# Kernel optimization log

Hardware: AMD Instinct MI355X
Metric: run time of the kernel (lower is better)

Reference implementation:

```python
import jax, jax.numpy as jnp
import numpy as np

B, T, IN, H = 1024, 200, 128, 128

def _linear_params(key, out_dim, in_dim):
    kw, kb = jax.random.split(key)
    bound = 1.0 / np.sqrt(in_dim)
    w = jax.random.uniform(kw, (out_dim, in_dim), jnp.float32, -bound, bound)
    b = jax.random.uniform(kb, (out_dim,), jnp.float32, -bound, bound)
    return w, b

def setup_inputs() -> dict:
    key = jax.random.key(0)
    ks = jax.random.split(key, 10)
    targets = jax.random.normal(ks[0], (B, T, IN), jnp.float32)
    history_states = jax.random.normal(ks[1], (B, T, H), jnp.float32)
    W_w, W_b = _linear_params(ks[2], H, IN)
    xu_w, xu_b = _linear_params(ks[3], H, H)
    hu_w, hu_b = _linear_params(ks[4], H, H)
    xr_w, xr_b = _linear_params(ks[5], H, H)
    hr_w, hr_b = _linear_params(ks[6], H, H)
    xg_w, xg_b = _linear_params(ks[7], H, H)
    hg_w, hg_b = _linear_params(ks[8], H, H)
    ln2_w, ln2_b = _linear_params(ks[9], H, IN + H)
    return dict(targets=targets, history_states=history_states,
                W_w=W_w, W_b=W_b, xu_w=xu_w, xu_b=xu_b, hu_w=hu_w, hu_b=hu_b,
                xr_w=xr_w, xr_b=xr_b, hr_w=hr_w, hr_b=hr_b,
                xg_w=xg_w, xg_b=xg_b, hg_w=hg_w, hg_b=hg_b,
                ln2_w=ln2_w, ln2_b=ln2_b)

def reference(targets, history_states, W_w, W_b, xu_w, xu_b, hu_w, hu_b,
              xr_w, xr_b, hr_w, hr_b, xg_w, xg_b, hg_w, hg_b, ln2_w, ln2_b):
    # attention weights: softmax over time of <W(targets), history>
    aw = jnp.einsum('bti,hi->bth', targets, W_w) + W_b            # [B,T,H]
    att = jax.nn.softmax(jnp.sum(aw * history_states, -1, keepdims=True), axis=1)  # [B,T,1]

    # precompute input-side projections as big GEMMs (same math as per-step Linear)
    xu = jnp.einsum('bth,oh->bto', history_states, xu_w) + xu_b   # [B,T,H]
    xr = jnp.einsum('bth,oh->bto', history_states, xr_w) + xr_b
    xg = jnp.einsum('bth,oh->bto', history_states, xg_w) + xg_b

    def step(h, xs):
        xu_t, xr_t, xg_t, a_t = xs                                 # [B,H],[B,H],[B,H],[B,1]
        u = jax.nn.sigmoid(xu_t + h @ hu_w.T + hu_b) * a_t
        r = jax.nn.sigmoid(xr_t + h @ hr_w.T + hr_b)
        g = jnp.tanh(xg_t + r * (h @ hg_w.T + hg_b))
        h = (1.0 - u) * h + u * g
        return h, None

    h0 = jnp.zeros((targets.shape[0], hu_w.shape[0]), targets.dtype)
    # scan over time: move T to leading axis
    xs = (jnp.swapaxes(xu, 0, 1), jnp.swapaxes(xr, 0, 1),
          jnp.swapaxes(xg, 0, 1), jnp.swapaxes(att, 0, 1))
    h, _ = jax.lax.scan(step, h0, xs)

    out = jnp.concatenate([h, targets[:, 0]], axis=-1) @ ln2_w.T + ln2_b
    return out
```

## Files before the change

### kernel.cpp

```cpp
#include <hip/hip_runtime.h>

#define B_ 1024
#define T_ 200
#define H_ 128

typedef __attribute__((ext_vector_type(8))) short short8;
typedef __attribute__((ext_vector_type(4))) float f32x4;

#define MFMA(a, b, c) __builtin_amdgcn_mfma_f32_16x16x32_bf16((a), (b), (c), 0, 0, 0)

static __device__ __forceinline__ short f2bf(float f) {
  unsigned u = __float_as_uint(f);
  u += 0x7fffu + ((u >> 16) & 1u);
  return (short)(u >> 16);
}
static __device__ __forceinline__ float bf2f(short s) {
  return __uint_as_float(((unsigned)(unsigned short)s) << 16);
}
static __device__ __forceinline__ unsigned pack2bf_rne(float a, float b) {
  unsigned ua = __float_as_uint(a);
  ua += 0x7fffu + ((ua >> 16) & 1u);
  unsigned ub = __float_as_uint(b);
  ub += 0x7fffu + ((ub >> 16) & 1u);
  return (ua >> 16) | (ub & 0xFFFF0000u);
}
static __device__ __forceinline__ unsigned pack2bf_trunc(float a, float b) {
  return (__float_as_uint(a) >> 16) | (__float_as_uint(b) & 0xFFFF0000u);
}
static __device__ __forceinline__ float rcp_f(float x) { return __builtin_amdgcn_rcpf(x); }
static __device__ __forceinline__ void ck_barrier() {
  asm volatile("s_waitcnt lgkmcnt(0)\n\ts_barrier" ::: "memory");
}

__global__ __launch_bounds__(512, 1) void proj_scores_kernel(
    const float* __restrict__ tgt, const float* __restrict__ hist,
    const float* __restrict__ Ww, const float* __restrict__ Wb,
    float* __restrict__ scores, short* __restrict__ histbf) {
  const int tc = blockIdx.x, bb = blockIdx.y;
  const int nt = (tc == 12) ? 8 : 16;
  const int t0 = tc * 16;
  const int tid = threadIdx.x;
  const int lane = tid & 63, w = tid >> 6;
  const int n = lane & 15, q = lane >> 4;

  __shared__ short tgt_hi[2][16 * 128];
  __shared__ short tgt_lo[2][16 * 128];
  __shared__ float hist_f[2][16 * 132];
  __shared__ float sp[16 * 8];

  short8 whi[4], wlo[4];
  f32x4 wb4;
  {
    const int o = w * 16 + n;
#pragma unroll
    for (int ks = 0; ks < 4; ++ks) {
      const float* p = Ww + o * H_ + ks * 32 + q * 8;
      short8 h, l;
#pragma unroll
      for (int j = 0; j < 8; ++j) {
        float f = p[j];
        short hv = f2bf(f);
        h[j] = hv;
        l[j] = f2bf(f - bf2f(hv));
      }
      whi[ks] = h;
      wlo[ks] = l;
    }
    wb4 = *(const f32x4*)(Wb + w * 16 + q * 4);
  }

  const int sm = tid >> 5, cs = tid & 31;
  const int g = cs >> 1, half = cs & 1;
  const int spos16 = sm * 128 + ((g ^ (sm & 7)) * 8) + half * 4;
  const int sposf = sm * 132 + cs * 4;
  const size_t rowbase = ((size_t)(bb * 16 + sm) * T_) * H_ + cs * 4;

  const int cu = tid;
  const int cks = cu >> 7, crem = cu & 127, cwl = crem >> 1, chalf = crem & 1;
  const int crow = cwl & 15, ckb = cks * 32 + (cwl >> 4) * 8 + chalf * 4;

  float4 hv = *(const float4*)(hist + rowbase + (size_t)t0 * H_);
  float4 tv = *(const float4*)(tgt + rowbase + (size_t)t0 * H_);
  {
    *(float4*)&hist_f[0][sposf] = hv;
    uint2 hi, lo;
    hi.x = pack2bf_rne(tv.x, tv.y);
    hi.y = pack2bf_rne(tv.z, tv.w);
    lo.x = pack2bf_rne(tv.x - bf2f((short)(hi.x)), tv.y - bf2f((short)(hi.x >> 16)));
    lo.y = pack2bf_rne(tv.z - bf2f((short)(hi.y)), tv.w - bf2f((short)(hi.y >> 16)));
    *(uint2*)&tgt_hi[0][spos16] = hi;
    *(uint2*)&tgt_lo[0][spos16] = lo;
  }
  ck_barrier();

  for (int tl = 0; tl < nt; ++tl) {
    const int cur = tl & 1, nxt = cur ^ 1;
    const bool have_next = (tl + 1 < nt);
    if (have_next) {
      hv = *(const float4*)(hist + rowbase + (size_t)(t0 + tl + 1) * H_);
      tv = *(const float4*)(tgt + rowbase + (size_t)(t0 + tl + 1) * H_);
    }
    f32x4 s1 = {0, 0, 0, 0}, s2 = {0, 0, 0, 0}, s3 = {0, 0, 0, 0};
#pragma unroll
    for (int ks = 0; ks < 4; ++ks) {
      const int fp = n * 128 + ((ks * 4 + q) ^ (n & 7)) * 8;
      short8 ahi = *(short8*)&tgt_hi[cur][fp];
      short8 alo = *(short8*)&tgt_lo[cur][fp];
      s1 = MFMA(whi[ks], ahi, s1);
      s2 = MFMA(wlo[ks], ahi, s2);
      s3 = MFMA(whi[ks], alo, s3);
    }
    {
      f32x4 hv4 = *(const f32x4*)&hist_f[cur][n * 132 + w * 16 + q * 4];
      float v = (s1[0] + s2[0] + s3[0] + wb4[0]) * hv4[0];
      v += (s1[1] + s2[1] + s3[1] + wb4[1]) * hv4[1];
      v += (s1[2] + s2[2] + s3[2] + wb4[2]) * hv4[2];
      v += (s1[3] + s2[3] + s3[3] + wb4[3]) * hv4[3];
      v += __shfl_xor(v, 16);
      v += __shfl_xor(v, 32);
      if (lane < 16) sp[n * 8 + w] = v;
    }
    if (histbf != nullptr) {
      const float* src = &hist_f[cur][crow * 132 + ckb];
      uint2 u;
      u.x = pack2bf_rne(src[0], src[1]);
      u.y = pack2bf_rne(src[2], src[3]);
      const size_t sb = (((size_t)(bb * T_ + t0 + tl) * 4) + cks) * 512 + cwl * 8 + chalf * 4;
      *(uint2*)(histbf + sb) = u;
    }
    if (have_next) {
      *(float4*)&hist_f[nxt][sposf] = hv;
      uint2 hi, lo;
      hi.x = pack2bf_rne(tv.x, tv.y);
      hi.y = pack2bf_rne(tv.z, tv.w);
      lo.x = pack2bf_rne(tv.x - bf2f((short)(hi.x)), tv.y - bf2f((short)(hi.x >> 16)));
      lo.y = pack2bf_rne(tv.z - bf2f((short)(hi.y)), tv.w - bf2f((short)(hi.y >> 16)));
      *(uint2*)&tgt_hi[nxt][spos16] = hi;
      *(uint2*)&tgt_lo[nxt][spos16] = lo;
    }
    ck_barrier();
    if (tid < 16) {
      float s = 0.0f;
#pragma unroll
      for (int ww = 0; ww < 8; ++ww) s += sp[tid * 8 + ww];
      scores[(size_t)(bb * 16 + tid) * T_ + (t0 + tl)] = s;
    }
    ck_barrier();
  }
}

__global__ __launch_bounds__(256, 4) void softmax_kernel(float* __restrict__ att) {
  const int b = blockIdx.x, tid = threadIdx.x;
  const int lane = tid & 63, wave = tid >> 6;
  __shared__ float red[8];
  float v = (tid < T_) ? att[(size_t)b * T_ + tid] : -3.0e38f;
  float mx = v;
#pragma unroll
  for (int d = 1; d < 64; d <<= 1) mx = fmaxf(mx, __shfl_xor(mx, d));
  if (lane == 0) red[wave] = mx;
  __syncthreads();
  mx = fmaxf(fmaxf(red[0], red[1]), fmaxf(red[2], red[3]));
  float e = (tid < T_) ? __expf(v - mx) : 0.0f;
  float sm = e;
#pragma unroll
  for (int d = 1; d < 64; d <<= 1) sm += __shfl_xor(sm, d);
  if (lane == 0) red[4 + wave] = sm;
  __syncthreads();
  sm = red[4] + red[5] + red[6] + red[7];
  if (tid < T_) att[(size_t)b * T_ + tid] = e / sm;
}

template <bool DIRECT>
__global__ __launch_bounds__(512, 2) void scan3_kernel(
    const float* __restrict__ hist,
    const float* __restrict__ xu_w, const float* __restrict__ xu_b,
    const float* __restrict__ hu_w, const float* __restrict__ hu_b,
    const float* __restrict__ xr_w, const float* __restrict__ xr_b,
    const float* __restrict__ hr_w, const float* __restrict__ hr_b,
    const float* __restrict__ xg_w, const float* __restrict__ xg_b,
    const float* __restrict__ hg_w, const float* __restrict__ hg_b,
    const float* __restrict__ att, const short* __restrict__ histbf,
    float* __restrict__ h_out) {
  const int tid = threadIdx.x;
  const int lane = tid & 63, w = tid >> 6;
  const int n = lane & 15, q = lane >> 4;
  const int bb = blockIdx.x, r0 = bb * 16;
  const int o = w * 16 + n;
  const int ob = w * 16 + q * 4;

  __shared__ short hbuf[2][16 * 128];
  __shared__ short xbuf[2][16 * 128];

  short8 wf[6][4];
  {
    const float* Wm[6] = {xu_w, hu_w, xr_w, hr_w, xg_w, hg_w};
#pragma unroll
    for (int M = 0; M < 6; ++M)
#pragma unroll
      for (int ks = 0; ks < 4; ++ks) {
        const float* p = Wm[M] + o * H_ + ks * 32 + q * 8;
        short8 v;
#pragma unroll
        for (int j = 0; j < 8; ++j) v[j] = f2bf(p[j]);
        wf[M][ks] = v;
      }
  }
  const f32x4 bu4 = *(const f32x4*)(xu_b + ob) + *(const f32x4*)(hu_b + ob);
  const f32x4 br4 = *(const f32x4*)(xr_b + ob) + *(const f32x4*)(hr_b + ob);
  const f32x4 bxg4 = *(const f32x4*)(xg_b + ob);
  const f32x4 bhg4 = *(const f32x4*)(hg_b + ob);

  for (int i = tid; i < 16 * 128; i += 512) hbuf[0][i] = 0;

  typedef union { uint4 u; short8 s; } frag_u;
  frag_u xp[2][4];
  const short* px = histbf + ((size_t)bb * T_ * 4) * 512 + (size_t)lane * 8;
  const int sm = tid >> 5, cs = tid & 31;
  const int xpos = sm * 128 + (((cs >> 1) ^ (sm & 7)) * 8) + (cs & 1) * 4;
  const float* hrow = hist + ((size_t)(r0 + sm) * T_) * H_ + cs * 4;
  float4 xnext;

  if constexpr (DIRECT) {
#pragma unroll
    for (int s = 0; s < 2; ++s)
#pragma unroll
      for (int ks = 0; ks < 4; ++ks)
        xp[s][ks].u = *(const uint4*)(px + (size_t)(s * 4 + ks) * 512);
  } else {
    float4 a = *(const float4*)hrow;
    uint2 u;
    u.x = pack2bf_rne(a.x, a.y);
    u.y = pack2bf_rne(a.z, a.w);
    *(uint2*)&xbuf[0][xpos] = u;
    xnext = *(const float4*)(hrow + H_);
  }

  float ap2[2];
  const float* pa = att + (size_t)(r0 + n) * T_;
  ap2[0] = pa[0];
  ap2[1] = pa[1];

  float hreg[4] = {0.0f, 0.0f, 0.0f, 0.0f};
  const int wri = n * 128 + (((w * 2 + (q >> 1)) ^ (n & 7)) * 8) + (q & 1) * 4;
  ck_barrier();

#pragma unroll 2
  for (int t = 0; t < T_; ++t) {
    const int cur = t & 1, nxt = cur ^ 1;
    short8 ha[4];
#pragma unroll
    for (int ks = 0; ks < 4; ++ks)
      ha[ks] = *(short8*)&hbuf[cur][n * 128 + ((ks * 4 + q) ^ (n & 7)) * 8];
    short8 xa[4];
    if constexpr (DIRECT) {
#pragma unroll
      for (int ks = 0; ks < 4; ++ks) xa[ks] = xp[cur][ks].s;
    } else {
#pragma unroll
      for (int ks = 0; ks < 4; ++ks)
        xa[ks] = *(short8*)&xbuf[cur][n * 128 + ((ks * 4 + q) ^ (n & 7)) * 8];
    }
    f32x4 axu = {0, 0, 0, 0}, ahu = {0, 0, 0, 0}, axr = {0, 0, 0, 0},
          ahr = {0, 0, 0, 0}, axg = {0, 0, 0, 0}, ahg = {0, 0, 0, 0};
#pragma unroll
    for (int ks = 0; ks < 4; ++ks) {
      axu = MFMA(wf[0][ks], xa[ks], axu);
      axr = MFMA(wf[2][ks], xa[ks], axr);
      axg = MFMA(wf[4][ks], xa[ks], axg);
    }
#pragma unroll
    for (int ks = 0; ks < 4; ++ks) {
      ahu = MFMA(wf[1][ks], ha[ks], ahu);
      ahr = MFMA(wf[3][ks], ha[ks], ahr);
      ahg = MFMA(wf[5][ks], ha[ks], ahg);
    }
    const int tp = (t + 2 < T_) ? t + 2 : T_ - 1;
    if constexpr (DIRECT) {
#pragma unroll
      for (int ks = 0; ks < 4; ++ks)
        xp[cur][ks].u = *(const uint4*)(px + (size_t)(tp * 4 + ks) * 512);
    } else {
      uint2 u;
      u.x = pack2bf_rne(xnext.x, xnext.y);
      u.y = pack2bf_rne(xnext.z, xnext.w);
      *(uint2*)&xbuf[nxt][xpos] = u;
      xnext = *(const float4*)(hrow + (size_t)tp * H_);
    }
    const float at = ap2[cur];
    ap2[cur] = pa[tp];
    float hn[4];
#pragma unroll
    for (int r = 0; r < 4; ++r) {
      const float su = axu[r] + ahu[r] + bu4[r];
      const float u = at * rcp_f(1.0f + __expf(-su));
      const float sr = axr[r] + ahr[r] + br4[r];
      const float rr = rcp_f(1.0f + __expf(-sr));
      const float sg = (axg[r] + bxg4[r]) + rr * (ahg[r] + bhg4[r]);
      const float g = 2.0f * rcp_f(1.0f + __expf(-2.0f * sg)) - 1.0f;
      hn[r] = hreg[r] + u * (g - hreg[r]);
      hreg[r] = hn[r];
    }
    uint2 up;
    up.x = pack2bf_trunc(hn[0], hn[1]);
    up.y = pack2bf_trunc(hn[2], hn[3]);
    *(uint2*)&hbuf[nxt][wri] = up;
    if (t == T_ - 1) {
      f32x4 hv = {hn[0], hn[1], hn[2], hn[3]};
      *(f32x4*)(h_out + (size_t)(r0 + n) * H_ + ob) = hv;
    }
    ck_barrier();
  }
}

__global__ __launch_bounds__(256, 4) void final_kernel(
    const float* __restrict__ tgt, const float* __restrict__ hfin,
    const float* __restrict__ w, const float* __restrict__ bias,
    float* __restrict__ out) {
  const int b = blockIdx.x, tid = threadIdx.x;
  const int o = tid >> 1, half = tid & 1;
  const float* src = half ? (tgt + (size_t)b * (T_ * H_)) : (hfin + (size_t)b * H_);
  const float* wrow = w + o * 256 + half * 128;
  float acc = 0.0f;
#pragma unroll 8
  for (int k = 0; k < 128; k += 4) {
    float4 sv = *(const float4*)(src + k);
    float4 wv = *(const float4*)(wrow + k);
    acc += sv.x * wv.x + sv.y * wv.y + sv.z * wv.z + sv.w * wv.w;
  }
  acc += __shfl_xor(acc, 1);
  if (half == 0) out[(size_t)b * H_ + o] = acc + bias[o];
}

extern "C" void kernel_launch(void* const* d_in, const int* in_sizes, int n_in,
                              void* d_out, int out_size, void* d_ws, size_t ws_size,
                              hipStream_t stream) {
  const float* targets = (const float*)d_in[0];
  const float* history = (const float*)d_in[1];
  const float* W_w = (const float*)d_in[2];
  const float* W_b = (const float*)d_in[3];
  const float* xu_w = (const float*)d_in[4];
  const float* xu_b = (const float*)d_in[5];
  const float* hu_w = (const float*)d_in[6];
  const float* hu_b = (const float*)d_in[7];
  const float* xr_w = (const float*)d_in[8];
  const float* xr_b = (const float*)d_in[9];
  const float* hr_w = (const float*)d_in[10];
  const float* hr_b = (const float*)d_in[11];
  const float* xg_w = (const float*)d_in[12];
  const float* xg_b = (const float*)d_in[13];
  const float* hg_w = (const float*)d_in[14];
  const float* hg_b = (const float*)d_in[15];
  const float* ln2_w = (const float*)d_in[16];
  const float* ln2_b = (const float*)d_in[17];
  float* out = (float*)d_out;

  float* att = (float*)d_ws;
  float* hfin = att + (size_t)B_ * T_;
  const size_t fixed = (size_t)B_ * T_ * 4 + (size_t)B_ * H_ * 4;
  const size_t histbf_bytes = (size_t)64 * T_ * 4 * 512 * 8 * 2;
  short* histbf = (ws_size >= fixed + histbf_bytes)
                      ? (short*)((char*)d_ws + fixed)
                      : nullptr;

  proj_scores_kernel<<<dim3(13, 64), dim3(512), 0, stream>>>(
      targets, history, W_w, W_b, att, histbf);
  softmax_kernel<<<dim3(B_), dim3(256), 0, stream>>>(att);
  if (histbf) {
    scan3_kernel<true><<<dim3(64), dim3(512), 0, stream>>>(
        history, xu_w, xu_b, hu_w, hu_b, xr_w, xr_b, hr_w, hr_b,
        xg_w, xg_b, hg_w, hg_b, att, histbf, hfin);
  } else {
    scan3_kernel<false><<<dim3(64), dim3(512), 0, stream>>>(
        history, xu_w, xu_b, hu_w, hu_b, xr_w, xr_b, hr_w, hr_b,
        xg_w, xg_b, hg_w, hg_b, att, histbf, hfin);
  }
  final_kernel<<<dim3(B_), dim3(256), 0, stream>>>(targets, hfin, ln2_w, ln2_b, out);
}
```

Before: 490.6 us.

## Software-pipeline input projections one step ahead of recurrent MFMAs in scan

In the direct path, the input-side projections (xu, xr, xg) for step t+1 are now computed during step t and kept in a double-buffered accumulator, with biases folded into the accumulator init. Only the recurrent h-side MFMAs stay on the serial dependency chain, and the prefetch distance grows to t+3. Launch bounds drop from 2 to 1 block per SIMD to give the extra live accumulators register room, and the final h store moves out of the loop. This costs occupancy and register pressure in exchange for a shorter critical path per step.

Result: faster. 471.4 us (-3.9%).

```diff
diff --git a/kernel.cpp b/kernel.cpp
--- a/kernel.cpp
+++ b/kernel.cpp
@@ -171,7 +171,7 @@
 }
 
 template <bool DIRECT>
-__global__ __launch_bounds__(512, 2) void scan3_kernel(
+__global__ __launch_bounds__(512, 1) void scan3_kernel(
     const float* __restrict__ hist,
     const float* __restrict__ xu_w, const float* __restrict__ xu_b,
     const float* __restrict__ hu_w, const float* __restrict__ hu_b,
@@ -220,12 +220,28 @@
   const float* hrow = hist + ((size_t)(r0 + sm) * T_) * H_ + cs * 4;
   float4 xnext;
 
+  f32x4 xq[2][3];
+
   if constexpr (DIRECT) {
-#pragma unroll
-    for (int s = 0; s < 2; ++s)
-#pragma unroll
-      for (int ks = 0; ks < 4; ++ks)
-        xp[s][ks].u = *(const uint4*)(px + (size_t)(s * 4 + ks) * 512);
+    frag_u x0[4];
+#pragma unroll
+    for (int ks = 0; ks < 4; ++ks)
+      x0[ks].u = *(const uint4*)(px + (size_t)(0 * 4 + ks) * 512);
+#pragma unroll
+    for (int ks = 0; ks < 4; ++ks)
+      xp[1][ks].u = *(const uint4*)(px + (size_t)(1 * 4 + ks) * 512);
+#pragma unroll
+    for (int ks = 0; ks < 4; ++ks)
+      xp[0][ks].u = *(const uint4*)(px + (size_t)(2 * 4 + ks) * 512);
+    xq[0][0] = bu4;
+    xq[0][1] = br4;
+    xq[0][2] = bxg4;
+#pragma unroll
+    for (int ks = 0; ks < 4; ++ks) {
+      xq[0][0] = MFMA(wf[0][ks], x0[ks].s, xq[0][0]);
+      xq[0][1] = MFMA(wf[2][ks], x0[ks].s, xq[0][1]);
+      xq[0][2] = MFMA(wf[4][ks], x0[ks].s, xq[0][2]);
+    }
   } else {
     float4 a = *(const float4*)hrow;
     uint2 u;
@@ -251,51 +267,64 @@
 #pragma unroll
     for (int ks = 0; ks < 4; ++ks)
       ha[ks] = *(short8*)&hbuf[cur][n * 128 + ((ks * 4 + q) ^ (n & 7)) * 8];
-    short8 xa[4];
-    if constexpr (DIRECT) {
-#pragma unroll
-      for (int ks = 0; ks < 4; ++ks) xa[ks] = xp[cur][ks].s;
-    } else {
-#pragma unroll
-      for (int ks = 0; ks < 4; ++ks)
-        xa[ks] = *(short8*)&xbuf[cur][n * 128 + ((ks * 4 + q) ^ (n & 7)) * 8];
-    }
-    f32x4 axu = {0, 0, 0, 0}, ahu = {0, 0, 0, 0}, axr = {0, 0, 0, 0},
-          ahr = {0, 0, 0, 0}, axg = {0, 0, 0, 0}, ahg = {0, 0, 0, 0};
-#pragma unroll
-    for (int ks = 0; ks < 4; ++ks) {
-      axu = MFMA(wf[0][ks], xa[ks], axu);
-      axr = MFMA(wf[2][ks], xa[ks], axr);
-      axg = MFMA(wf[4][ks], xa[ks], axg);
-    }
+
+    f32x4 ahu = {0, 0, 0, 0}, ahr = {0, 0, 0, 0}, ahg = {0, 0, 0, 0};
 #pragma unroll
     for (int ks = 0; ks < 4; ++ks) {
       ahu = MFMA(wf[1][ks], ha[ks], ahu);
       ahr = MFMA(wf[3][ks], ha[ks], ahr);
       ahg = MFMA(wf[5][ks], ha[ks], ahg);
     }
-    const int tp = (t + 2 < T_) ? t + 2 : T_ - 1;
+
     if constexpr (DIRECT) {
+      xq[nxt][0] = bu4;
+      xq[nxt][1] = br4;
+      xq[nxt][2] = bxg4;
+#pragma unroll
+      for (int ks = 0; ks < 4; ++ks) {
+        short8 xs = xp[nxt][ks].s;
+        xq[nxt][0] = MFMA(wf[0][ks], xs, xq[nxt][0]);
+        xq[nxt][1] = MFMA(wf[2][ks], xs, xq[nxt][1]);
+        xq[nxt][2] = MFMA(wf[4][ks], xs, xq[nxt][2]);
+      }
+      const int tf = (t + 3 < T_) ? t + 3 : T_ - 1;
 #pragma unroll
       for (int ks = 0; ks < 4; ++ks)
-        xp[cur][ks].u = *(const uint4*)(px + (size_t)(tp * 4 + ks) * 512);
+        xp[nxt][ks].u = *(const uint4*)(px + (size_t)(tf * 4 + ks) * 512);
     } else {
+      short8 xa[4];
+#pragma unroll
+      for (int ks = 0; ks < 4; ++ks)
+        xa[ks] = *(short8*)&xbuf[cur][n * 128 + ((ks * 4 + q) ^ (n & 7)) * 8];
+      xq[cur][0] = bu4;
+      xq[cur][1] = br4;
+      xq[cur][2] = bxg4;
+#pragma unroll
+      for (int ks = 0; ks < 4; ++ks) {
+        xq[cur][0] = MFMA(wf[0][ks], xa[ks], xq[cur][0]);
+        xq[cur][1] = MFMA(wf[2][ks], xa[ks], xq[cur][1]);
+        xq[cur][2] = MFMA(wf[4][ks], xa[ks], xq[cur][2]);
+      }
+      const int tp = (t + 2 < T_) ? t + 2 : T_ - 1;
       uint2 u;
       u.x = pack2bf_rne(xnext.x, xnext.y);
       u.y = pack2bf_rne(xnext.z, xnext.w);
       *(uint2*)&xbuf[nxt][xpos] = u;
       xnext = *(const float4*)(hrow + (size_t)tp * H_);
     }
+
+    const int tp = (t + 2 < T_) ? t + 2 : T_ - 1;
     const float at = ap2[cur];
     ap2[cur] = pa[tp];
+
     float hn[4];
 #pragma unroll
     for (int r = 0; r < 4; ++r) {
-      const float su = axu[r] + ahu[r] + bu4[r];
+      const float su = xq[cur][0][r] + ahu[r];
       const float u = at * rcp_f(1.0f + __expf(-su));
-      const float sr = axr[r] + ahr[r] + br4[r];
+      const float sr = xq[cur][1][r] + ahr[r];
       const float rr = rcp_f(1.0f + __expf(-sr));
-      const float sg = (axg[r] + bxg4[r]) + rr * (ahg[r] + bhg4[r]);
+      const float sg = xq[cur][2][r] + rr * (ahg[r] + bhg4[r]);
       const float g = 2.0f * rcp_f(1.0f + __expf(-2.0f * sg)) - 1.0f;
       hn[r] = hreg[r] + u * (g - hreg[r]);
       hreg[r] = hn[r];
@@ -304,12 +333,11 @@
     up.x = pack2bf_trunc(hn[0], hn[1]);
     up.y = pack2bf_trunc(hn[2], hn[3]);
     *(uint2*)&hbuf[nxt][wri] = up;
-    if (t == T_ - 1) {
-      f32x4 hv = {hn[0], hn[1], hn[2], hn[3]};
-      *(f32x4*)(h_out + (size_t)(r0 + n) * H_ + ob) = hv;
-    }
     ck_barrier();
   }
+
+  f32x4 hv = {hreg[0], hreg[1], hreg[2], hreg[3]};
+  *(f32x4*)(h_out + (size_t)(r0 + n) * H_ + ob) = hv;
 }
 
 __global__ __launch_bounds__(256, 4) void final_kernel(
```
